# Performance work log

Hardware: AMD Instinct MI355X
Metric: run time of the kernel (lower is better)

Reference implementation:

```python
import jax, jax.numpy as jnp
import numpy as np

NEG_INF = -9e15  # matches the -9000000000000000.0 mask constant in the torch code
ALPHA = 0.2      # LeakyReLU negative slope


def setup_inputs() -> dict:
    key = jax.random.key(0)
    ks = jax.random.split(key, 8)
    N, F = 8192, 256
    h = jax.random.normal(ks[0], (N, F), dtype=jnp.float32)
    adj = jax.random.randint(ks[1], (N, N), 0, 2).astype(jnp.float32)
    W = jax.random.normal(ks[2], (F, F), dtype=jnp.float32) * 0.05
    a = jax.random.normal(ks[3], (2 * F, 1), dtype=jnp.float32) * 0.05
    w_ih = jax.random.normal(ks[4], (3 * F, F), dtype=jnp.float32) * 0.05
    w_hh = jax.random.normal(ks[5], (3 * F, F), dtype=jnp.float32) * 0.05
    b_ih = jax.random.normal(ks[6], (3 * F,), dtype=jnp.float32) * 0.05
    b_hh = jax.random.normal(ks[7], (3 * F,), dtype=jnp.float32) * 0.05
    return {"h": h, "adj": adj, "W": W, "a": a,
            "w_ih": w_ih, "w_hh": w_hh, "b_ih": b_ih, "b_hh": b_hh}


def reference(h, adj, W, a, w_ih, w_hh, b_ih, b_hh):
    F_out = W.shape[1]
    Wh = h @ W  # [N, F]
    # a_input @ a decomposes exactly: e_ij = leakyrelu(Wh_i . a[:F] + Wh_j . a[F:])
    src = Wh @ a[:F_out]   # [N, 1]
    dst = Wh @ a[F_out:]   # [N, 1]
    e = jax.nn.leaky_relu(src + dst.T, ALPHA)          # [N, N]
    att = jnp.where(adj > 0, e, NEG_INF)
    att = jax.nn.softmax(att, axis=1)                   # dropout: eval mode (identity)
    h_prime = att @ Wh                                  # [N, F]
    # torch GRUCell(h_prime, h)
    gi = h_prime @ w_ih.T + b_ih                        # [N, 3F]
    gh = h @ w_hh.T + b_hh
    i_r, i_z, i_n = jnp.split(gi, 3, axis=1)
    h_r, h_z, h_n = jnp.split(gh, 3, axis=1)
    r = jax.nn.sigmoid(i_r + h_r)
    z = jax.nn.sigmoid(i_z + h_z)
    n = jnp.tanh(i_n + r * h_n)
    return (1.0 - z) * n + z * h
```

## Files before the change

kernel.cpp:

```cpp
#include <hip/hip_runtime.h>

typedef __attribute__((ext_vector_type(8))) short bf16x8;
typedef __attribute__((ext_vector_type(4))) float f32x4;
typedef unsigned short u16;

#define NN 8192
#define FD 256

__device__ __forceinline__ u16 f2bf(float f) {
  union { float f; unsigned u; } v; v.f = f;
  unsigned r = v.u + 0x7FFF + ((v.u >> 16) & 1);
  return (u16)(r >> 16);
}

__global__ __launch_bounds__(256) void k_wh(const float* __restrict__ h,
                                            const float* __restrict__ W,
                                            const float* __restrict__ a,
                                            u16* __restrict__ whT,
                                            float* __restrict__ src,
                                            float* __restrict__ dst) {
  int tid = threadIdx.x;
  int lane = tid & 63;
  int wv = tid >> 6;
  int r0 = blockIdx.x * 64 + (wv >> 1) * 32;
  int c0 = blockIdx.y * 64 + (wv & 1) * 32;
  int lr = lane & 15;
  int q = lane >> 4;

  f32x4 acc[2][2] = {};
  for (int kk = 0; kk < FD; kk += 32) {
    int kb = kk + q * 8;
    bf16x8 av[2], bv[2];
#pragma unroll
    for (int m = 0; m < 2; m++) {
      const float* p = h + (size_t)(r0 + m * 16 + lr) * FD + kb;
      f32x4 x0 = *(const f32x4*)p;
      f32x4 x1 = *(const f32x4*)(p + 4);
      bf16x8 t;
      t[0] = (short)f2bf(x0[0]); t[1] = (short)f2bf(x0[1]);
      t[2] = (short)f2bf(x0[2]); t[3] = (short)f2bf(x0[3]);
      t[4] = (short)f2bf(x1[0]); t[5] = (short)f2bf(x1[1]);
      t[6] = (short)f2bf(x1[2]); t[7] = (short)f2bf(x1[3]);
      av[m] = t;
    }
#pragma unroll
    for (int n = 0; n < 2; n++) {
      int col = c0 + n * 16 + lr;
      const float* p = W + (size_t)kb * FD + col;
      bf16x8 t;
#pragma unroll
      for (int e = 0; e < 8; e++) t[e] = (short)f2bf(p[(size_t)e * FD]);
      bv[n] = t;
    }
#pragma unroll
    for (int m = 0; m < 2; m++)
#pragma unroll
      for (int n = 0; n < 2; n++)
        acc[m][n] = __builtin_amdgcn_mfma_f32_16x16x32_bf16(av[m], bv[n], acc[m][n], 0, 0, 0);
  }
#pragma unroll
  for (int m = 0; m < 2; m++)
#pragma unroll
    for (int n = 0; n < 2; n++) {
      int gc = c0 + n * 16 + lr;
      int gr = r0 + m * 16 + q * 4;
      ushort4 st;
      st.x = f2bf(acc[m][n][0]);
      st.y = f2bf(acc[m][n][1]);
      st.z = f2bf(acc[m][n][2]);
      st.w = f2bf(acc[m][n][3]);
      *(ushort4*)(whT + (size_t)gc * NN + gr) = st;
    }
  float aA0 = a[c0 + lr], aA1 = a[c0 + 16 + lr];
  float aB0 = a[256 + c0 + lr], aB1 = a[256 + c0 + 16 + lr];
#pragma unroll
  for (int m = 0; m < 2; m++)
#pragma unroll
    for (int j = 0; j < 4; j++) {
      float s1 = acc[m][0][j] * aA0 + acc[m][1][j] * aA1;
      float s2 = acc[m][0][j] * aB0 + acc[m][1][j] * aB1;
#pragma unroll
      for (int sh = 1; sh < 16; sh <<= 1) {
        s1 += __shfl_xor(s1, sh);
        s2 += __shfl_xor(s2, sh);
      }
      if (lr == 0) {
        int row = r0 + m * 16 + q * 4 + j;
        atomicAdd(&src[row], s1);
        atomicAdd(&dst[row], s2);
      }
    }
}

__global__ __launch_bounds__(256) void k_cast(const float* __restrict__ h,
                                              const float* __restrict__ wih,
                                              const float* __restrict__ whh,
                                              u16* __restrict__ hb,
                                              u16* __restrict__ wihb,
                                              u16* __restrict__ whhb) {
  int g = blockIdx.x * 256 + threadIdx.x;
  const int hG = NN * FD / 4;
  const int wG = 768 * FD / 4;
  const float* sp;
  u16* dp;
  int off;
  if (g < hG) { sp = h; dp = hb; off = g; }
  else if (g < hG + wG) { sp = wih; dp = wihb; off = g - hG; }
  else { sp = whh; dp = whhb; off = g - hG - wG; }
  f32x4 x = *(const f32x4*)(sp + (size_t)off * 4);
  ushort4 y;
  y.x = f2bf(x[0]); y.y = f2bf(x[1]); y.z = f2bf(x[2]); y.w = f2bf(x[3]);
  *(ushort4*)(dp + (size_t)off * 4) = y;
}

__global__ __launch_bounds__(512, 2) void k_att(const float* __restrict__ adj,
                                                const u16* __restrict__ whT,
                                                const float* __restrict__ src,
                                                const float* __restrict__ dst,
                                                u16* __restrict__ hpb) {
  __shared__ u16 pbuf[3][2048];
  __shared__ float dst_lds[8448];
  __shared__ float l_lds[32];

  const int tid = threadIdx.x;
  const int lane = tid & 63;
  const int w = tid >> 6;
  const int lr = lane & 15;
  const int q = lane >> 4;
  const int i0 = blockIdx.x * 32;

  const int pi = tid >> 4;
  const int j4 = (tid & 15) * 4;
  const int oW = j4 >> 3;
  const int pwoff = ((oW >> 2) * 2 + (pi >> 4)) * 512 + ((oW & 3) * 16 + (pi & 15)) * 8 + ((j4 >> 2) & 1) * 4;

  const float* adjT = adj + (size_t)(i0 + pi) * NN + j4;
  const float srcv = src[i0 + pi];
  float lsum = 0.f;

#pragma unroll
  for (int k = 0; k < 4; k++) {
    f32x4 v = *(const f32x4*)(dst + tid * 16 + k * 4);
    *(f32x4*)&dst_lds[tid * 16 + k * 4] = v;
  }
  __syncthreads();

  f32x4 acc[2][2] = {};
  bf16x8 A0[2][2], A1[2][2];
  f32x4 R0, R1;

#define LBAR asm volatile("s_waitcnt lgkmcnt(0)\n\ts_barrier" ::: "memory")
#define RLOAD(S, R) R = *(const f32x4*)(adjT + (size_t)(S) * 64);
#define ALOAD(S, A)                                                          \
  {                                                                          \
    _Pragma("unroll") for (int m = 0; m < 2; m++)                            \
    _Pragma("unroll") for (int kh = 0; kh < 2; kh++)                         \
      A[m][kh] = *(const bf16x8*)(whT + (size_t)(w * 32 + m * 16 + lr) * NN + (S) * 64 + kh * 32 + q * 8); \
  }
#define PSTEP(S, AR, WB)                                                     \
  {                                                                          \
    f32x4 dv = *(const f32x4*)&dst_lds[(S) * 64 + j4];                       \
    float p0, p1, p2, p3;                                                    \
    { float x = srcv + dv[0]; x = fmaxf(x, 0.2f * x); p0 = AR[0] * __expf(x); } \
    { float x = srcv + dv[1]; x = fmaxf(x, 0.2f * x); p1 = AR[1] * __expf(x); } \
    { float x = srcv + dv[2]; x = fmaxf(x, 0.2f * x); p2 = AR[2] * __expf(x); } \
    { float x = srcv + dv[3]; x = fmaxf(x, 0.2f * x); p3 = AR[3] * __expf(x); } \
    lsum += (p0 + p1) + (p2 + p3);                                           \
    ushort4 st;                                                              \
    st.x = f2bf(p0); st.y = f2bf(p1); st.z = f2bf(p2); st.w = f2bf(p3);      \
    *(ushort4*)&pbuf[WB][pwoff] = st;                                        \
  }
#define CMP(RB, A)                                                           \
  {                                                                          \
    _Pragma("unroll") for (int kh = 0; kh < 2; kh++)                         \
    _Pragma("unroll") for (int n = 0; n < 2; n++) {                          \
      bf16x8 pf = *(const bf16x8*)&pbuf[RB][(kh * 2 + n) * 512 + (q * 16 + lr) * 8]; \
      _Pragma("unroll") for (int m = 0; m < 2; m++)                          \
        acc[m][n] = __builtin_amdgcn_mfma_f32_16x16x32_bf16(A[m][kh], pf, acc[m][n], 0, 0, 0); \
    }                                                                        \
  }

  RLOAD(0, R0);
  RLOAD(1, R1);
  ALOAD(0, A0);
  PSTEP(0, R0, 0);
  LBAR;

  int rb = 0, wb = 1;
  for (int t = 0; t < 128; t += 2) {
    if (t + 2 < 128) { RLOAD(t + 2, R0); }
    PSTEP(t + 1, R1, wb);
    ALOAD(t + 1, A1);
    CMP(rb, A0);
    LBAR;
    rb = wb; wb = (wb == 2) ? 0 : wb + 1;
    if (t + 3 < 128) { RLOAD(t + 3, R1); }
    if (t + 2 < 128) {
      PSTEP(t + 2, R0, wb);
      ALOAD(t + 2, A0);
    }
    CMP(rb, A1);
    LBAR;
    rb = wb; wb = (wb == 2) ? 0 : wb + 1;
  }
#undef LBAR
#undef RLOAD
#undef ALOAD
#undef PSTEP
#undef CMP

  lsum += __shfl_xor(lsum, 1);
  lsum += __shfl_xor(lsum, 2);
  lsum += __shfl_xor(lsum, 4);
  lsum += __shfl_xor(lsum, 8);
  if ((tid & 15) == 0) l_lds[pi] = lsum;
  __syncthreads();

  u16* ost = (u16*)dst_lds;
#pragma unroll
  for (int n = 0; n < 2; n++) {
    float inv = 1.0f / l_lds[n * 16 + lr];
#pragma unroll
    for (int m = 0; m < 2; m++) {
      ushort4 st;
      st.x = f2bf(acc[m][n][0] * inv);
      st.y = f2bf(acc[m][n][1] * inv);
      st.z = f2bf(acc[m][n][2] * inv);
      st.w = f2bf(acc[m][n][3] * inv);
      *(ushort4*)&ost[(n * 16 + lr) * 264 + w * 32 + m * 16 + q * 4] = st;
    }
  }
  __syncthreads();
  {
    int r = tid >> 4;
    int c = (tid & 15) * 16;
    bf16x8 v0 = *(const bf16x8*)&ost[r * 264 + c];
    bf16x8 v1 = *(const bf16x8*)&ost[r * 264 + c + 8];
    *(bf16x8*)(hpb + (size_t)(i0 + r) * FD + c) = v0;
    *(bf16x8*)(hpb + (size_t)(i0 + r) * FD + c + 8) = v1;
  }
}

__global__ __launch_bounds__(256) void k_gru(const u16* __restrict__ hpb,
                                             const u16* __restrict__ hb,
                                             const u16* __restrict__ wihb,
                                             const u16* __restrict__ whhb,
                                             const float* __restrict__ bih,
                                             const float* __restrict__ bhh,
                                             const float* __restrict__ h,
                                             float* __restrict__ out) {
  int tid = threadIdx.x;
  int lane = tid & 63;
  int wv = tid >> 6;
  int i0 = blockIdx.x * 32;
  int lr = lane & 15;
  int q = lane >> 4;
  int c = blockIdx.y * 64 + wv * 16 + lr;
  f32x4 gi[3][2] = {};
  f32x4 gh[3][2] = {};
  for (int kk = 0; kk < FD; kk += 32) {
    int kb = kk + q * 8;
    bf16x8 ap[2], ah[2], bi[3], bh[3];
#pragma unroll
    for (int m = 0; m < 2; m++) {
      ap[m] = *(const bf16x8*)(hpb + (size_t)(i0 + m * 16 + lr) * FD + kb);
      ah[m] = *(const bf16x8*)(hb + (size_t)(i0 + m * 16 + lr) * FD + kb);
    }
#pragma unroll
    for (int g = 0; g < 3; g++) {
      bi[g] = *(const bf16x8*)(wihb + (size_t)(g * 256 + c) * FD + kb);
      bh[g] = *(const bf16x8*)(whhb + (size_t)(g * 256 + c) * FD + kb);
    }
#pragma unroll
    for (int g = 0; g < 3; g++)
#pragma unroll
      for (int m = 0; m < 2; m++) {
        gi[g][m] = __builtin_amdgcn_mfma_f32_16x16x32_bf16(ap[m], bi[g], gi[g][m], 0, 0, 0);
        gh[g][m] = __builtin_amdgcn_mfma_f32_16x16x32_bf16(ah[m], bh[g], gh[g][m], 0, 0, 0);
      }
  }
  float bir = bih[c], biz = bih[256 + c], bin = bih[512 + c];
  float bhr = bhh[c], bhz = bhh[256 + c], bhn = bhh[512 + c];
#pragma unroll
  for (int m = 0; m < 2; m++)
#pragma unroll
    for (int j = 0; j < 4; j++) {
      int row = i0 + m * 16 + q * 4 + j;
      float rv = gi[0][m][j] + bir + gh[0][m][j] + bhr;
      float zv = gi[1][m][j] + biz + gh[1][m][j] + bhz;
      float r = 1.f / (1.f + __expf(-rv));
      float z = 1.f / (1.f + __expf(-zv));
      float nx = gi[2][m][j] + bin + r * (gh[2][m][j] + bhn);
      float n = 1.f - 2.f / (__expf(2.f * nx) + 1.f);
      float hv = h[(size_t)row * FD + c];
      out[(size_t)row * FD + c] = (1.f - z) * n + z * hv;
    }
}

extern "C" void kernel_launch(void* const* d_in, const int* in_sizes, int n_in,
                              void* d_out, int out_size, void* d_ws, size_t ws_size,
                              hipStream_t stream) {
  const float* h   = (const float*)d_in[0];
  const float* adj = (const float*)d_in[1];
  const float* W   = (const float*)d_in[2];
  const float* a   = (const float*)d_in[3];
  const float* wih = (const float*)d_in[4];
  const float* whh = (const float*)d_in[5];
  const float* bih = (const float*)d_in[6];
  const float* bhh = (const float*)d_in[7];
  float* out = (float*)d_out;

  char* ws = (char*)d_ws;
  u16* whT  = (u16*)(ws);
  u16* hpb  = (u16*)(ws + 4194304);
  u16* hb   = (u16*)(ws + 8388608);
  u16* wihb = (u16*)(ws + 12582912);
  u16* whhb = (u16*)(ws + 12976128);
  float* srcv = (float*)(ws + 13369344);
  float* dstv = (float*)(ws + 13402112);

  hipMemsetAsync(ws + 13369344, 0, 65536, stream);
  k_wh<<<dim3(128, 4), 256, 0, stream>>>(h, W, a, whT, srcv, dstv);
  k_cast<<<2432, 256, 0, stream>>>(h, wih, whh, hb, wihb, whhb);
  k_att<<<256, 512, 0, stream>>>(adj, whT, srcv, dstv, hpb);
  k_gru<<<dim3(256, 4), 256, 0, stream>>>(hpb, hb, wihb, whhb, bih, bhh, h, out);
}
```

Before: 236.0 us.

## Split attention over key chunks with 128-row tiles and atomic partial sums

The attention kernel now gives each block 128 query rows and one quarter of the key dimension, so each block loads the bf16 Wh^T tiles once for four times as many rows. It uses a swizzled LDS probability buffer and accumulates unnormalised outputs and row sums into global fp32 buffers with atomics. A new normalisation kernel divides by the row sums and writes the bf16 output. The separate cast kernel is removed, and the GRU converts h and its weights to bf16 inline. The trade-offs are a large memset, many fp32 atomics, one extra kernel launch, and lower occupancy (launch bounds 512,1).

```diff
diff --git a/kernel.cpp b/kernel.cpp
--- a/kernel.cpp
+++ b/kernel.cpp
@@ -11,6 +11,17 @@
   union { float f; unsigned u; } v; v.f = f;
   unsigned r = v.u + 0x7FFF + ((v.u >> 16) & 1);
   return (u16)(r >> 16);
+}
+
+__device__ __forceinline__ bf16x8 ldcvt8(const float* __restrict__ p) {
+  f32x4 x0 = *(const f32x4*)p;
+  f32x4 x1 = *(const f32x4*)(p + 4);
+  bf16x8 t;
+  t[0] = (short)f2bf(x0[0]); t[1] = (short)f2bf(x0[1]);
+  t[2] = (short)f2bf(x0[2]); t[3] = (short)f2bf(x0[3]);
+  t[4] = (short)f2bf(x1[0]); t[5] = (short)f2bf(x1[1]);
+  t[6] = (short)f2bf(x1[2]); t[7] = (short)f2bf(x1[3]);
+  return t;
 }
 
 __global__ __launch_bounds__(256) void k_wh(const float* __restrict__ h,
@@ -32,17 +43,8 @@
     int kb = kk + q * 8;
     bf16x8 av[2], bv[2];
 #pragma unroll
-    for (int m = 0; m < 2; m++) {
-      const float* p = h + (size_t)(r0 + m * 16 + lr) * FD + kb;
-      f32x4 x0 = *(const f32x4*)p;
-      f32x4 x1 = *(const f32x4*)(p + 4);
-      bf16x8 t;
-      t[0] = (short)f2bf(x0[0]); t[1] = (short)f2bf(x0[1]);
-      t[2] = (short)f2bf(x0[2]); t[3] = (short)f2bf(x0[3]);
-      t[4] = (short)f2bf(x1[0]); t[5] = (short)f2bf(x1[1]);
-      t[6] = (short)f2bf(x1[2]); t[7] = (short)f2bf(x1[3]);
-      av[m] = t;
-    }
+    for (int m = 0; m < 2; m++)
+      av[m] = ldcvt8(h + (size_t)(r0 + m * 16 + lr) * FD + kb);
 #pragma unroll
     for (int n = 0; n < 2; n++) {
       int col = c0 + n * 16 + lr;
@@ -92,162 +94,144 @@
     }
 }
 
-__global__ __launch_bounds__(256) void k_cast(const float* __restrict__ h,
-                                              const float* __restrict__ wih,
-                                              const float* __restrict__ whh,
-                                              u16* __restrict__ hb,
-                                              u16* __restrict__ wihb,
-                                              u16* __restrict__ whhb) {
-  int g = blockIdx.x * 256 + threadIdx.x;
-  const int hG = NN * FD / 4;
-  const int wG = 768 * FD / 4;
-  const float* sp;
-  u16* dp;
-  int off;
-  if (g < hG) { sp = h; dp = hb; off = g; }
-  else if (g < hG + wG) { sp = wih; dp = wihb; off = g - hG; }
-  else { sp = whh; dp = whhb; off = g - hG - wG; }
-  f32x4 x = *(const f32x4*)(sp + (size_t)off * 4);
-  ushort4 y;
-  y.x = f2bf(x[0]); y.y = f2bf(x[1]); y.z = f2bf(x[2]); y.w = f2bf(x[3]);
-  *(ushort4*)(dp + (size_t)off * 4) = y;
-}
-
-__global__ __launch_bounds__(512, 2) void k_att(const float* __restrict__ adj,
+__global__ __launch_bounds__(512, 1) void k_att(const float* __restrict__ adj,
                                                 const u16* __restrict__ whT,
                                                 const float* __restrict__ src,
                                                 const float* __restrict__ dst,
-                                                u16* __restrict__ hpb) {
-  __shared__ u16 pbuf[3][2048];
-  __shared__ float dst_lds[8448];
-  __shared__ float l_lds[32];
+                                                float* __restrict__ hp,
+                                                float* __restrict__ lg) {
+  __shared__ u16 pbuf[3][8192];
+  __shared__ float dst_lds[2048];
+  __shared__ float lred[4][128];
 
   const int tid = threadIdx.x;
   const int lane = tid & 63;
   const int w = tid >> 6;
   const int lr = lane & 15;
   const int q = lane >> 4;
-  const int i0 = blockIdx.x * 32;
-
-  const int pi = tid >> 4;
-  const int j4 = (tid & 15) * 4;
-  const int oW = j4 >> 3;
-  const int pwoff = ((oW >> 2) * 2 + (pi >> 4)) * 512 + ((oW & 3) * 16 + (pi & 15)) * 8 + ((j4 >> 2) & 1) * 4;
-
-  const float* adjT = adj + (size_t)(i0 + pi) * NN + j4;
+  const int bid = blockIdx.x;
+  const int jh = bid & 3;
+  const int i0 = (bid >> 2) * 128;
+  const int jb = jh * 2048;
+
+  const int pi = tid & 127;
+  const int jg = tid >> 7;
+  const float* adjP = adj + (size_t)(i0 + pi) * NN + jb + jg * 16;
   const float srcv = src[i0 + pi];
+  const int c0 = w * 32;
+  const u16* wp = whT + (size_t)(c0 + lr) * NN + jb + q * 8;
+  const int pw0 = (pi * 64 + jg * 16) ^ ((pi & 7) << 3);
+  const int pw1 = (pi * 64 + jg * 16 + 8) ^ ((pi & 7) << 3);
+
+  f32x4 ar0[4], ar1[4];
+  bf16x8 B0[2][2], B1[2][2];
+  f32x4 acc[8][2] = {};
   float lsum = 0.f;
 
-#pragma unroll
-  for (int k = 0; k < 4; k++) {
-    f32x4 v = *(const f32x4*)(dst + tid * 16 + k * 4);
-    *(f32x4*)&dst_lds[tid * 16 + k * 4] = v;
-  }
+  *(f32x4*)&dst_lds[tid * 4] = *(const f32x4*)(dst + jb + tid * 4);
+
+#define AL(S, AR)                                                              \
+  { _Pragma("unroll") for (int v = 0; v < 4; v++)                              \
+      AR[v] = *(const f32x4*)(adjP + (size_t)(S) * 64 + v * 4); }
+#define BL(S, B)                                                               \
+  { _Pragma("unroll") for (int kh = 0; kh < 2; kh++)                           \
+    _Pragma("unroll") for (int n = 0; n < 2; n++)                              \
+      B[kh][n] = *(const bf16x8*)(wp + (size_t)n * 16 * NN + (S) * 64 + kh * 32); }
+#define PS(S, AR, WB)                                                          \
+  {                                                                            \
+    u16 pv[16];                                                                \
+    _Pragma("unroll") for (int v = 0; v < 4; v++)                              \
+      _Pragma("unroll") for (int e = 0; e < 4; e++) {                          \
+        float x = srcv + dst_lds[(S) * 64 + jg * 16 + v * 4 + e];              \
+        x = fmaxf(x, 0.2f * x);                                                \
+        float p = AR[v][e] * __expf(x);                                        \
+        lsum += p;                                                             \
+        pv[v * 4 + e] = f2bf(p);                                               \
+      }                                                                        \
+    bf16x8 s0, s1;                                                             \
+    _Pragma("unroll") for (int e = 0; e < 8; e++) {                            \
+      s0[e] = (short)pv[e]; s1[e] = (short)pv[8 + e];                          \
+    }                                                                          \
+    *(bf16x8*)&pbuf[WB][pw0] = s0;                                             \
+    *(bf16x8*)&pbuf[WB][pw1] = s1;                                             \
+  }
+#define CMPS(RB, B)                                                            \
+  {                                                                            \
+    _Pragma("unroll") for (int m = 0; m < 8; m++)                              \
+      _Pragma("unroll") for (int kh = 0; kh < 2; kh++) {                       \
+        bf16x8 pf = *(const bf16x8*)&pbuf[RB][((m * 16 + lr) * 64 + kh * 32 + q * 8) ^ ((lr & 7) << 3)]; \
+        acc[m][0] = __builtin_amdgcn_mfma_f32_16x16x32_bf16(pf, B[kh][0], acc[m][0], 0, 0, 0); \
+        acc[m][1] = __builtin_amdgcn_mfma_f32_16x16x32_bf16(pf, B[kh][1], acc[m][1], 0, 0, 0); \
+      }                                                                        \
+  }
+#define LBAR asm volatile("s_waitcnt lgkmcnt(0)\n\ts_barrier" ::: "memory")
+
+  AL(0, ar0);
+  AL(1, ar1);
+  BL(0, B0);
   __syncthreads();
-
-  f32x4 acc[2][2] = {};
-  bf16x8 A0[2][2], A1[2][2];
-  f32x4 R0, R1;
-
-#define LBAR asm volatile("s_waitcnt lgkmcnt(0)\n\ts_barrier" ::: "memory")
-#define RLOAD(S, R) R = *(const f32x4*)(adjT + (size_t)(S) * 64);
-#define ALOAD(S, A)                                                          \
-  {                                                                          \
-    _Pragma("unroll") for (int m = 0; m < 2; m++)                            \
-    _Pragma("unroll") for (int kh = 0; kh < 2; kh++)                         \
-      A[m][kh] = *(const bf16x8*)(whT + (size_t)(w * 32 + m * 16 + lr) * NN + (S) * 64 + kh * 32 + q * 8); \
-  }
-#define PSTEP(S, AR, WB)                                                     \
-  {                                                                          \
-    f32x4 dv = *(const f32x4*)&dst_lds[(S) * 64 + j4];                       \
-    float p0, p1, p2, p3;                                                    \
-    { float x = srcv + dv[0]; x = fmaxf(x, 0.2f * x); p0 = AR[0] * __expf(x); } \
-    { float x = srcv + dv[1]; x = fmaxf(x, 0.2f * x); p1 = AR[1] * __expf(x); } \
-    { float x = srcv + dv[2]; x = fmaxf(x, 0.2f * x); p2 = AR[2] * __expf(x); } \
-    { float x = srcv + dv[3]; x = fmaxf(x, 0.2f * x); p3 = AR[3] * __expf(x); } \
-    lsum += (p0 + p1) + (p2 + p3);                                           \
-    ushort4 st;                                                              \
-    st.x = f2bf(p0); st.y = f2bf(p1); st.z = f2bf(p2); st.w = f2bf(p3);      \
-    *(ushort4*)&pbuf[WB][pwoff] = st;                                        \
-  }
-#define CMP(RB, A)                                                           \
-  {                                                                          \
-    _Pragma("unroll") for (int kh = 0; kh < 2; kh++)                         \
-    _Pragma("unroll") for (int n = 0; n < 2; n++) {                          \
-      bf16x8 pf = *(const bf16x8*)&pbuf[RB][(kh * 2 + n) * 512 + (q * 16 + lr) * 8]; \
-      _Pragma("unroll") for (int m = 0; m < 2; m++)                          \
-        acc[m][n] = __builtin_amdgcn_mfma_f32_16x16x32_bf16(A[m][kh], pf, acc[m][n], 0, 0, 0); \
-    }                                                                        \
-  }
-
-  RLOAD(0, R0);
-  RLOAD(1, R1);
-  ALOAD(0, A0);
-  PSTEP(0, R0, 0);
+  PS(0, ar0, 0);
   LBAR;
 
   int rb = 0, wb = 1;
-  for (int t = 0; t < 128; t += 2) {
-    if (t + 2 < 128) { RLOAD(t + 2, R0); }
-    PSTEP(t + 1, R1, wb);
-    ALOAD(t + 1, A1);
-    CMP(rb, A0);
+  for (int t = 0; t < 32; t += 2) {
+    if (t + 2 < 32) AL(t + 2, ar0);
+    PS(t + 1, ar1, wb);
+    BL(t + 1, B1);
+    CMPS(rb, B0);
     LBAR;
     rb = wb; wb = (wb == 2) ? 0 : wb + 1;
-    if (t + 3 < 128) { RLOAD(t + 3, R1); }
-    if (t + 2 < 128) {
-      PSTEP(t + 2, R0, wb);
-      ALOAD(t + 2, A0);
-    }
-    CMP(rb, A1);
+    if (t + 3 < 32) AL(t + 3, ar1);
+    if (t + 2 < 32) {
+      PS(t + 2, ar0, wb);
+      BL(t + 2, B0);
+    }
+    CMPS(rb, B1);
     LBAR;
     rb = wb; wb = (wb == 2) ? 0 : wb + 1;
   }
+#undef AL
+#undef BL
+#undef PS
+#undef CMPS
 #undef LBAR
-#undef RLOAD
-#undef ALOAD
-#undef PSTEP
-#undef CMP
-
-  lsum += __shfl_xor(lsum, 1);
-  lsum += __shfl_xor(lsum, 2);
-  lsum += __shfl_xor(lsum, 4);
-  lsum += __shfl_xor(lsum, 8);
-  if ((tid & 15) == 0) l_lds[pi] = lsum;
+
+  lred[jg][pi] = lsum;
   __syncthreads();
-
-  u16* ost = (u16*)dst_lds;
-#pragma unroll
-  for (int n = 0; n < 2; n++) {
-    float inv = 1.0f / l_lds[n * 16 + lr];
-#pragma unroll
-    for (int m = 0; m < 2; m++) {
-      ushort4 st;
-      st.x = f2bf(acc[m][n][0] * inv);
-      st.y = f2bf(acc[m][n][1] * inv);
-      st.z = f2bf(acc[m][n][2] * inv);
-      st.w = f2bf(acc[m][n][3] * inv);
-      *(ushort4*)&ost[(n * 16 + lr) * 264 + w * 32 + m * 16 + q * 4] = st;
-    }
-  }
-  __syncthreads();
-  {
-    int r = tid >> 4;
-    int c = (tid & 15) * 16;
-    bf16x8 v0 = *(const bf16x8*)&ost[r * 264 + c];
-    bf16x8 v1 = *(const bf16x8*)&ost[r * 264 + c + 8];
-    *(bf16x8*)(hpb + (size_t)(i0 + r) * FD + c) = v0;
-    *(bf16x8*)(hpb + (size_t)(i0 + r) * FD + c + 8) = v1;
-  }
+  if (tid < 128) {
+    float l = (lred[0][tid] + lred[1][tid]) + (lred[2][tid] + lred[3][tid]);
+    atomicAdd(&lg[i0 + tid], l);
+  }
+#pragma unroll
+  for (int m = 0; m < 8; m++)
+#pragma unroll
+    for (int n = 0; n < 2; n++)
+#pragma unroll
+      for (int j = 0; j < 4; j++)
+        atomicAdd(&hp[(size_t)(i0 + m * 16 + q * 4 + j) * FD + c0 + n * 16 + lr],
+                  acc[m][n][j]);
+}
+
+__global__ __launch_bounds__(256) void k_norm(const float* __restrict__ hp,
+                                              const float* __restrict__ lg,
+                                              u16* __restrict__ hpb) {
+  int g = blockIdx.x * 1024 + threadIdx.x * 4;
+  f32x4 v = *(const f32x4*)(hp + g);
+  float inv = 1.0f / lg[g >> 8];
+  ushort4 st;
+  st.x = f2bf(v[0] * inv);
+  st.y = f2bf(v[1] * inv);
+  st.z = f2bf(v[2] * inv);
+  st.w = f2bf(v[3] * inv);
+  *(ushort4*)(hpb + g) = st;
 }
 
 __global__ __launch_bounds__(256) void k_gru(const u16* __restrict__ hpb,
-                                             const u16* __restrict__ hb,
-                                             const u16* __restrict__ wihb,
-                                             const u16* __restrict__ whhb,
+                                             const float* __restrict__ h,
+                                             const float* __restrict__ wih,
+                                             const float* __restrict__ whh,
                                              const float* __restrict__ bih,
                                              const float* __restrict__ bhh,
-                                             const float* __restrict__ h,
                                              float* __restrict__ out) {
   int tid = threadIdx.x;
   int lane = tid & 63;
@@ -264,12 +248,12 @@
 #pragma unroll
     for (int m = 0; m < 2; m++) {
       ap[m] = *(const bf16x8*)(hpb + (size_t)(i0 + m * 16 + lr) * FD + kb);
-      ah[m] = *(const bf16x8*)(hb + (size_t)(i0 + m * 16 + lr) * FD + kb);
+      ah[m] = ldcvt8(h + (size_t)(i0 + m * 16 + lr) * FD + kb);
     }
 #pragma unroll
     for (int g = 0; g < 3; g++) {
-      bi[g] = *(const bf16x8*)(wihb + (size_t)(g * 256 + c) * FD + kb);
-      bh[g] = *(const bf16x8*)(whhb + (size_t)(g * 256 + c) * FD + kb);
+      bi[g] = ldcvt8(wih + (size_t)(g * 256 + c) * FD + kb);
+      bh[g] = ldcvt8(whh + (size_t)(g * 256 + c) * FD + kb);
     }
 #pragma unroll
     for (int g = 0; g < 3; g++)
@@ -311,17 +295,17 @@
   float* out = (float*)d_out;
 
   char* ws = (char*)d_ws;
-  u16* whT  = (u16*)(ws);
-  u16* hpb  = (u16*)(ws + 4194304);
-  u16* hb   = (u16*)(ws + 8388608);
-  u16* wihb = (u16*)(ws + 12582912);
-  u16* whhb = (u16*)(ws + 12976128);
-  float* srcv = (float*)(ws + 13369344);
-  float* dstv = (float*)(ws + 13402112);
-
-  hipMemsetAsync(ws + 13369344, 0, 65536, stream);
+  u16* whT   = (u16*)(ws);
+  u16* hpb   = (u16*)(ws);
+  float* hp  = (float*)(ws + 4194304);
+  float* lg  = (float*)(ws + 12582912);
+  float* srcv = (float*)(ws + 12615680);
+  float* dstv = (float*)(ws + 12648448);
+  (void)ws_size;
+
+  hipMemsetAsync(ws + 4194304, 0, 8486912, stream);
   k_wh<<<dim3(128, 4), 256, 0, stream>>>(h, W, a, whT, srcv, dstv);
-  k_cast<<<2432, 256, 0, stream>>>(h, wih, whh, hb, wihb, whhb);
-  k_att<<<256, 512, 0, stream>>>(adj, whT, srcv, dstv, hpb);
-  k_gru<<<dim3(256, 4), 256, 0, stream>>>(hpb, hb, wihb, whhb, bih, bhh, h, out);
-}
+  k_att<<<256, 512, 0, stream>>>(adj, whT, srcv, dstv, hp, lg);
+  k_norm<<<2048, 256, 0, stream>>>(hp, lg, hpb);
+  k_gru<<<dim3(256, 4), 256, 0, stream>>>(hpb, h, wih, whh, bih, bhh, out);
+}
```

New measurement: 209.1 us. 1.13x faster.
